# Kernel tuning notes

Measured on AMD Instinct MI355X. Metric: run time of the kernel, lower is better.

Reference implementation:

```python
import jax, jax.numpy as jnp
import numpy as np

N_HEAD = 4
D_MODEL = 128
D_K = D_MODEL // N_HEAD
N = 65536


def setup_inputs() -> dict:
    key = jax.random.key(0)
    ks = jax.random.split(key, 9)
    s = 1.0 / np.sqrt(D_MODEL)
    return {
        "query": jax.random.normal(ks[0], (N, D_MODEL), jnp.float32),
        "key": jax.random.normal(ks[1], (N, D_MODEL), jnp.float32),
        "value": jax.random.normal(ks[2], (N, D_MODEL), jnp.float32),
        "Wq": jax.random.normal(ks[3], (D_MODEL, D_MODEL), jnp.float32) * s,
        "bq": jax.random.normal(ks[4], (D_MODEL,), jnp.float32) * s,
        "Wk": jax.random.normal(ks[5], (D_MODEL, D_MODEL), jnp.float32) * s,
        "bk": jax.random.normal(ks[6], (D_MODEL,), jnp.float32) * s,
        "Wv": jax.random.normal(ks[7], (D_MODEL, D_MODEL), jnp.float32) * s,
        "bv": jax.random.normal(ks[8], (D_MODEL,), jnp.float32) * s,
    }


def _proj(x, W, b):
    # nn.Linear: x @ W.T + b, then view(N, n_head, d_k).transpose(0, 1) -> (h, N, d_k)
    y = x @ W.T + b
    return jnp.transpose(y.reshape(-1, N_HEAD, D_K), (1, 0, 2))


def reference(query, key, value, Wq, bq, Wk, bk, Wv, bv):
    n = query.shape[0]
    q = _proj(query, Wq, bq)  # (h, N, d_k)
    k = _proj(key, Wk, bk)
    v = _proj(value, Wv, bv)
    # galerkin linear attention: p_attn = (K^T V) / seq_len, out = Q @ p_attn
    p_attn = jnp.einsum("hnd,hne->hde", k, v) / n  # (h, d_k, d_k)
    x = jnp.einsum("hnd,hde->hne", q, p_attn)  # (h, N, d_k)
    # faithful to x.transpose(1,2).contiguous().view(bsz, -1, n_head*d_k)
    att_output = jnp.transpose(x, (0, 2, 1)).reshape(n, -1, N_HEAD * D_K)  # (N, 1, d_model)
    return att_output, p_attn
```

## Files before the change

kernel.cpp:

```cpp
#include <hip/hip_runtime.h>

typedef __attribute__((ext_vector_type(8))) short short8;
typedef __attribute__((ext_vector_type(4))) float f32x4;

#define WS_CKV  0
#define WS_SKEY 16384
#define WS_SVAL 16512
#define WS_W2T  16640
#define WS_B2   24832

#define SCR_CS  4194304

__device__ inline ushort f2bf(float f) {
    uint u = __float_as_uint(f);
    return (ushort)((u + 0x7FFFu + ((u >> 16) & 1u)) >> 16);
}
__device__ inline uint pack_bf16(float a, float b) {
    return (uint)f2bf(a) | ((uint)f2bf(b) << 16);
}
__device__ inline float bf2f(ushort u) { return __uint_as_float(((uint)u) << 16); }

__global__ __launch_bounds__(512, 4) void kernelA(const float* __restrict__ key,
                                                  const float* __restrict__ value,
                                                  float* __restrict__ outbuf) {
    __shared__ float lk[2][32 * 128];
    __shared__ float lv[2][32 * 128];
    __shared__ float red[256];

    const int tid = threadIdx.x;
    const int i0 = (tid >> 5) * 8;
    const int j0 = (tid & 31) * 4;
    const int row0 = blockIdx.x * 128;

    const float4* __restrict__ k4 = (const float4*)key;
    const float4* __restrict__ v4 = (const float4*)value;

    float acc[8][4];
#pragma unroll
    for (int a = 0; a < 8; ++a)
#pragma unroll
        for (int b = 0; b < 4; ++b) acc[a][b] = 0.f;

    float sk[4] = {0.f, 0.f, 0.f, 0.f};
    float sv[4] = {0.f, 0.f, 0.f, 0.f};

    float4 rk[2], rv[2];
    {
        const int g = row0 * 32;
        rk[0] = k4[g + tid]; rk[1] = k4[g + tid + 512];
        rv[0] = v4[g + tid]; rv[1] = v4[g + tid + 512];
        ((float4*)lk[0])[tid] = rk[0]; ((float4*)lk[0])[tid + 512] = rk[1];
        ((float4*)lv[0])[tid] = rv[0]; ((float4*)lv[0])[tid + 512] = rv[1];
#pragma unroll
        for (int q = 0; q < 2; ++q) {
            sk[0] += rk[q].x; sk[1] += rk[q].y; sk[2] += rk[q].z; sk[3] += rk[q].w;
            sv[0] += rv[q].x; sv[1] += rv[q].y; sv[2] += rv[q].z; sv[3] += rv[q].w;
        }
    }
    __syncthreads();

    for (int t = 0; t < 4; ++t) {
        const int cur = t & 1;
        if (t < 3) {
            const int g = (row0 + (t + 1) * 32) * 32;
            rk[0] = k4[g + tid]; rk[1] = k4[g + tid + 512];
            rv[0] = v4[g + tid]; rv[1] = v4[g + tid + 512];
        }
#pragma unroll 4
        for (int kk = 0; kk < 32; ++kk) {
            float ka[8], vb[4];
            *(float4*)&ka[0] = *(const float4*)&lk[cur][kk * 128 + i0];
            *(float4*)&ka[4] = *(const float4*)&lk[cur][kk * 128 + i0 + 4];
            *(float4*)&vb[0] = *(const float4*)&lv[cur][kk * 128 + j0];
#pragma unroll
            for (int a = 0; a < 8; ++a)
#pragma unroll
                for (int b = 0; b < 4; ++b)
                    acc[a][b] = fmaf(ka[a], vb[b], acc[a][b]);
        }
        if (t < 3) {
            const int nxt = cur ^ 1;
            ((float4*)lk[nxt])[tid] = rk[0]; ((float4*)lk[nxt])[tid + 512] = rk[1];
            ((float4*)lv[nxt])[tid] = rv[0]; ((float4*)lv[nxt])[tid + 512] = rv[1];
#pragma unroll
            for (int q = 0; q < 2; ++q) {
                sk[0] += rk[q].x; sk[1] += rk[q].y; sk[2] += rk[q].z; sk[3] += rk[q].w;
                sv[0] += rv[q].x; sv[1] += rv[q].y; sv[2] += rv[q].z; sv[3] += rv[q].w;
            }
            __syncthreads();
        }
    }

    if (tid < 256) red[tid] = 0.f;
    __syncthreads();
    const int cg = (tid & 31) * 4;
#pragma unroll
    for (int a = 0; a < 4; ++a) {
        atomicAdd(&red[cg + a], sk[a]);
        atomicAdd(&red[128 + cg + a], sv[a]);
    }
    __syncthreads();

    ushort* __restrict__ tile = (ushort*)outbuf + (size_t)blockIdx.x * 16384;
#pragma unroll
    for (int a = 0; a < 8; ++a) {
        uint2 s;
        s.x = pack_bf16(acc[a][0], acc[a][1]);
        s.y = pack_bf16(acc[a][2], acc[a][3]);
        *(uint2*)&tile[(i0 + a) * 128 + j0] = s;
    }
    if (tid < 256) outbuf[SCR_CS + blockIdx.x * 256 + tid] = red[tid];
}

__global__ __launch_bounds__(512) void kernelR(const float* __restrict__ outbuf,
                                               float* __restrict__ ws) {
    __shared__ float red[8][64];
    const int tid = threadIdx.x;
    const int b = blockIdx.x;
    const int lane = tid & 63;
    const int g = tid >> 6;
    const int p0 = g * 64;

    float s[8];
#pragma unroll
    for (int c = 0; c < 8; ++c) s[c] = 0.f;

    if (b < 256) {
        const ushort* __restrict__ tile = (const ushort*)outbuf;
        const int e = b * 64 + lane;
        for (int r = 0; r < 8; ++r) {
#pragma unroll
            for (int c = 0; c < 8; ++c)
                s[c] += bf2f(tile[(size_t)(p0 + c * 8 + r) * 16384 + e]);
        }
    } else {
        const int e = (b - 256) * 64 + lane;
        for (int r = 0; r < 8; ++r) {
#pragma unroll
            for (int c = 0; c < 8; ++c)
                s[c] += outbuf[SCR_CS + (p0 + c * 8 + r) * 256 + e];
        }
    }
    red[g][lane] = ((s[0] + s[1]) + (s[2] + s[3])) + ((s[4] + s[5]) + (s[6] + s[7]));
    __syncthreads();
    if (tid < 64) {
        float r = ((red[0][lane] + red[1][lane]) + (red[2][lane] + red[3][lane])) +
                  ((red[4][lane] + red[5][lane]) + (red[6][lane] + red[7][lane]));
        if (b < 256) ws[b * 64 + lane] = r;
        else ws[WS_SKEY + (b - 256) * 64 + lane] = r;
    }
}

__global__ __launch_bounds__(512) void kernelB(const float* __restrict__ Wk, const float* __restrict__ bk,
                                               const float* __restrict__ Wv, const float* __restrict__ bv,
                                               const float* __restrict__ Wq, const float* __restrict__ bq,
                                               float* __restrict__ ws, float* __restrict__ out) {
    __shared__ float ckv[128 * 132];
    __shared__ float wvT[128 * 32];
    __shared__ float wk_s[32 * 132];
    __shared__ float wq_s[32 * 132];
    __shared__ float Tl[128 * 32];
    __shared__ float pl[32 * 32];
    __shared__ float skey[128], sval[128];
    __shared__ float bk_s[32], bv_s[32], bq_s[32];
    __shared__ float wvec[32], uvec[32];

    const int tid = threadIdx.x;
    const int h = blockIdx.x;

    const float4* __restrict__ ws4 = (const float4*)ws;
    const float4* __restrict__ Wk4 = (const float4*)Wk;
    const float4* __restrict__ Wq4 = (const float4*)Wq;
    const float4* __restrict__ Wv4 = (const float4*)Wv;

#pragma unroll
    for (int q = 0; q < 8; ++q) {
        const int idx = tid + 512 * q;
        float4 v = ws4[(WS_CKV >> 2) + idx];
        *(float4*)&ckv[(idx >> 5) * 132 + (idx & 31) * 4] = v;
    }
#pragma unroll
    for (int q = 0; q < 2; ++q) {
        const int idx = tid + 512 * q;
        float4 a = Wk4[h * 1024 + idx];
        float4 b = Wq4[h * 1024 + idx];
        *(float4*)&wk_s[(idx >> 5) * 132 + (idx & 31) * 4] = a;
        *(float4*)&wq_s[(idx >> 5) * 132 + (idx & 31) * 4] = b;
    }
#pragma unroll
    for (int q = 0; q < 2; ++q) {
        const int f = tid + 512 * q;
        const int e = f >> 5;
        const int c = (f & 31) * 4;
        float4 v = Wv4[h * 1024 + f];
        wvT[(c + 0) * 32 + e] = v.x;
        wvT[(c + 1) * 32 + e] = v.y;
        wvT[(c + 2) * 32 + e] = v.z;
        wvT[(c + 3) * 32 + e] = v.w;
    }
    if (tid < 128) { skey[tid] = ws[WS_SKEY + tid]; sval[tid] = ws[WS_SVAL + tid]; }
    else if (tid >= 256 && tid < 288) {
        const int u = tid - 256;
        bk_s[u] = bk[h * 32 + u]; bv_s[u] = bv[h * 32 + u]; bq_s[u] = bq[h * 32 + u];
    }
    __syncthreads();

    {
        const int i = tid >> 2;
        const int e0 = (tid & 3) * 8;
        float accT8[8];
#pragma unroll
        for (int e = 0; e < 8; ++e) accT8[e] = 0.f;
        for (int j = 0; j < 128; ++j) {
            const float cv = ckv[i * 132 + j];
            const float* wr = &wvT[j * 32 + e0];
#pragma unroll
            for (int e = 0; e < 8; ++e) accT8[e] = fmaf(cv, wr[e], accT8[e]);
        }
#pragma unroll
        for (int e = 0; e < 8; e += 4)
            *(float4*)&Tl[i * 32 + e0 + e] = make_float4(accT8[e], accT8[e+1], accT8[e+2], accT8[e+3]);

        if (tid < 32) {
            float u = 0.f;
            for (int j = 0; j < 128; ++j) u = fmaf(wvT[j * 32 + tid], sval[j], u);
            uvec[tid] = u;
        } else if (tid < 64) {
            const int a = tid - 32;
            float w = 0.f;
            for (int i2 = 0; i2 < 128; ++i2) w = fmaf(wk_s[a * 132 + i2], skey[i2], w);
            wvec[a] = w;
        }
    }
    __syncthreads();

    {
        const int d = tid >> 4;
        const int e2 = (tid & 15) * 2;
        float pa = 0.f, pb = 0.f;
        for (int i2 = 0; i2 < 128; ++i2) {
            const float wkv = wk_s[d * 132 + i2];
            pa = fmaf(wkv, Tl[i2 * 32 + e2], pa);
            pb = fmaf(wkv, Tl[i2 * 32 + e2 + 1], pb);
        }
        const float p0 = (pa + wvec[d] * bv_s[e2] + bk_s[d] * uvec[e2] +
                          65536.f * bk_s[d] * bv_s[e2]) * (1.f / 65536.f);
        const float p1 = (pb + wvec[d] * bv_s[e2 + 1] + bk_s[d] * uvec[e2 + 1] +
                          65536.f * bk_s[d] * bv_s[e2 + 1]) * (1.f / 65536.f);
        pl[d * 32 + e2] = p0; pl[d * 32 + e2 + 1] = p1;
        *(float2*)&out[8388608 + h * 1024 + d * 32 + e2] = make_float2(p0, p1);
    }
    __syncthreads();

    {
        const int k = tid >> 2;
        const int e0 = (tid & 3) * 8;
        float accW[8];
#pragma unroll
        for (int e = 0; e < 8; ++e) accW[e] = 0.f;
        for (int d = 0; d < 32; ++d) {
            const float wq = wq_s[d * 132 + k];
            const float* pr = &pl[d * 32 + e0];
#pragma unroll
            for (int e = 0; e < 8; ++e) accW[e] = fmaf(wq, pr[e], accW[e]);
        }
        ushort* __restrict__ w2t = (ushort*)(ws + WS_W2T);
#pragma unroll
        for (int e = 0; e < 8; ++e)
            w2t[(h * 32 + e0 + e) * 128 + k] = f2bf(accW[e]);

        if (tid < 32) {
            float b2v = 0.f;
#pragma unroll
            for (int d = 0; d < 32; ++d) b2v = fmaf(bq_s[d], pl[d * 32 + tid], b2v);
            ws[WS_B2 + h * 32 + tid] = b2v;
        }
    }
}

__global__ __launch_bounds__(256, 2) void kernelC(const float* __restrict__ query,
                                                  const float* __restrict__ ws,
                                                  float* __restrict__ out) {
    __shared__ __align__(16) ushort qs[128 * 136];
    __shared__ __align__(16) ushort w2s[128 * 136];
    __shared__ float b2s[128];

    const int tid = threadIdx.x;
    const int lane = tid & 63;
    const int w = tid >> 6;
    const int wr = w >> 1, wc = w & 1;
    const int rowbase = blockIdx.x * 128;

    {
        const float4* __restrict__ q4 = (const float4*)query;
        const int r = tid >> 1, half = tid & 1;
        const int gbase = (rowbase + r) * 32 + half * 16;
#pragma unroll
        for (int m = 0; m < 8; ++m) {
            float4 f0 = q4[gbase + m * 2], f1 = q4[gbase + m * 2 + 1];
            uint4 pk;
            pk.x = pack_bf16(f0.x, f0.y); pk.y = pack_bf16(f0.z, f0.w);
            pk.z = pack_bf16(f1.x, f1.y); pk.w = pack_bf16(f1.z, f1.w);
            *(uint4*)&qs[r * 136 + half * 64 + m * 8] = pk;
        }
    }
    {
        const uint4* __restrict__ wsrc = (const uint4*)((const ushort*)(ws + WS_W2T));
        const int c = tid >> 1, half = tid & 1;
#pragma unroll
        for (int m = 0; m < 8; ++m) {
            uint4 v = wsrc[c * 16 + half * 8 + m];
            *(uint4*)&w2s[c * 136 + half * 64 + m * 8] = v;
        }
    }
    if (tid < 32) ((float4*)b2s)[tid] = ((const float4*)(ws + WS_B2))[tid];
    __syncthreads();

    short8 bfrag[4][4];
#pragma unroll
    for (int ct = 0; ct < 4; ++ct)
#pragma unroll
        for (int ks = 0; ks < 4; ++ks)
            bfrag[ct][ks] = *(const short8*)&w2s[(wc * 64 + ct * 16 + (lane & 15)) * 136 + ks * 32 + (lane >> 4) * 8];

    f32x4 acc[4][4];
#pragma unroll
    for (int rt = 0; rt < 4; ++rt)
#pragma unroll
        for (int ct = 0; ct < 4; ++ct) acc[rt][ct] = (f32x4){0.f, 0.f, 0.f, 0.f};

#pragma unroll
    for (int ks = 0; ks < 4; ++ks) {
        short8 af[4];
#pragma unroll
        for (int rt = 0; rt < 4; ++rt)
            af[rt] = *(const short8*)&qs[(wr * 64 + rt * 16 + (lane & 15)) * 136 + ks * 32 + (lane >> 4) * 8];
#pragma unroll
        for (int rt = 0; rt < 4; ++rt)
#pragma unroll
            for (int ct = 0; ct < 4; ++ct)
                acc[rt][ct] = __builtin_amdgcn_mfma_f32_16x16x32_bf16(af[rt], bfrag[ct][ks], acc[rt][ct], 0, 0, 0);
    }
    __syncthreads();

    float* tmp = (float*)qs;
#pragma unroll
    for (int cp = 0; cp < 4; ++cp) {
        if (wc == (cp >> 1)) {
#pragma unroll
            for (int rt = 0; rt < 4; ++rt)
#pragma unroll
                for (int tc = 0; tc < 2; ++tc) {
                    const int ct = (cp & 1) * 2 + tc;
                    const int cl = tc * 16 + (lane & 15);
                    const int r = wr * 64 + rt * 16 + (lane >> 4) * 4;
                    *(f32x4*)&tmp[cl * 132 + r] = acc[rt][ct];
                }
        }
        __syncthreads();
        {
            const int cl = tid >> 3;
            const int c = cp * 32 + cl;
            const float bb = b2s[c];
            float* __restrict__ col = out + (size_t)c * 65536 + rowbase;
#pragma unroll
            for (int ch = 0; ch < 4; ++ch) {
                const int r4 = (tid & 7) + ch * 8;
                float4 v = *(const float4*)&tmp[cl * 132 + r4 * 4];
                v.x += bb; v.y += bb; v.z += bb; v.w += bb;
                *(float4*)&col[r4 * 4] = v;
            }
        }
        __syncthreads();
    }
}

extern "C" void kernel_launch(void* const* d_in, const int* in_sizes, int n_in,
                              void* d_out, int out_size, void* d_ws, size_t ws_size,
                              hipStream_t stream) {
    const float* query = (const float*)d_in[0];
    const float* key   = (const float*)d_in[1];
    const float* value = (const float*)d_in[2];
    const float* Wq = (const float*)d_in[3];
    const float* bq = (const float*)d_in[4];
    const float* Wk = (const float*)d_in[5];
    const float* bk = (const float*)d_in[6];
    const float* Wv = (const float*)d_in[7];
    const float* bv = (const float*)d_in[8];
    float* out = (float*)d_out;
    float* ws  = (float*)d_ws;

    hipLaunchKernelGGL(kernelA, dim3(512), dim3(512), 0, stream, key, value, out);
    hipLaunchKernelGGL(kernelR, dim3(260), dim3(512), 0, stream, out, ws);
    hipLaunchKernelGGL(kernelB, dim3(4), dim3(512), 0, stream, Wk, bk, Wv, bv, Wq, bq, ws, out);
    hipLaunchKernelGGL(kernelC, dim3(512), dim3(256), 0, stream, query, ws, out);
}
```

Before: 197.4 us.

## Use bf16 MFMA for K^T V partial sums and coalesce staging loads

The per-block K^T·V partial products in kernelA now use bf16 MFMA 16x16x32 instead of scalar fp32 FMAs. K and V tiles are converted to bf16 and stored transposed in swizzled shared memory. The output tile is staged through shared memory so the global writes are coalesced uint4 stores. KernelC's query and weight loads into LDS are reorganized so consecutive threads read consecutive global addresses. This lowers ALU work and improves memory coalescing, at the cost of rounding K and V to bf16 before accumulation.

```diff
diff --git a/kernel.cpp b/kernel.cpp
--- a/kernel.cpp
+++ b/kernel.cpp
@@ -23,38 +23,48 @@
 __global__ __launch_bounds__(512, 4) void kernelA(const float* __restrict__ key,
                                                   const float* __restrict__ value,
                                                   float* __restrict__ outbuf) {
-    __shared__ float lk[2][32 * 128];
-    __shared__ float lv[2][32 * 128];
+    __shared__ __align__(16) ushort sm[4][128 * 40];
     __shared__ float red[256];
 
     const int tid = threadIdx.x;
-    const int i0 = (tid >> 5) * 8;
-    const int j0 = (tid & 31) * 4;
+    const int l = tid & 63;
+    const int w = tid >> 6;
+    const int rs = w * 16;
     const int row0 = blockIdx.x * 128;
 
     const float4* __restrict__ k4 = (const float4*)key;
     const float4* __restrict__ v4 = (const float4*)value;
 
-    float acc[8][4];
-#pragma unroll
-    for (int a = 0; a < 8; ++a)
-#pragma unroll
-        for (int b = 0; b < 4; ++b) acc[a][b] = 0.f;
+    const int n2 = tid >> 5;
+    const int i4 = tid & 31;
+    const int i0 = i4 * 4;
+    const int nds = n2 ^ (((i4 >> 1) & 3) << 2);
+
+    const int lr = l & 15;
+    const int g = l >> 4;
+
+    f32x4 acc[8];
+#pragma unroll
+    for (int c = 0; c < 8; ++c) acc[c] = (f32x4){0.f, 0.f, 0.f, 0.f};
 
     float sk[4] = {0.f, 0.f, 0.f, 0.f};
     float sv[4] = {0.f, 0.f, 0.f, 0.f};
 
-    float4 rk[2], rv[2];
-    {
-        const int g = row0 * 32;
-        rk[0] = k4[g + tid]; rk[1] = k4[g + tid + 512];
-        rv[0] = v4[g + tid]; rv[1] = v4[g + tid + 512];
-        ((float4*)lk[0])[tid] = rk[0]; ((float4*)lk[0])[tid + 512] = rk[1];
-        ((float4*)lv[0])[tid] = rv[0]; ((float4*)lv[0])[tid + 512] = rv[1];
-#pragma unroll
-        for (int q = 0; q < 2; ++q) {
-            sk[0] += rk[q].x; sk[1] += rk[q].y; sk[2] += rk[q].z; sk[3] += rk[q].w;
-            sv[0] += rv[q].x; sv[1] += rv[q].y; sv[2] += rv[q].z; sv[3] += rv[q].w;
+    float4 rka, rkb, rva, rvb;
+    {
+        const int gb = (row0 + 2 * n2) * 32 + i4;
+        rka = k4[gb]; rkb = k4[gb + 32];
+        rva = v4[gb]; rvb = v4[gb + 32];
+        uint* dk = (uint*)sm[0];
+        uint* dv = (uint*)sm[1];
+        const float* pa = (const float*)&rka; const float* pb = (const float*)&rkb;
+        const float* pc = (const float*)&rva; const float* pd = (const float*)&rvb;
+#pragma unroll
+        for (int q = 0; q < 4; ++q) {
+            dk[(i0 + q) * 20 + nds] = pack_bf16(pa[q], pb[q]);
+            dv[(i0 + q) * 20 + nds] = pack_bf16(pc[q], pd[q]);
+            sk[q] += pa[q] + pb[q];
+            sv[q] += pc[q] + pd[q];
         }
     }
     __syncthreads();
@@ -62,30 +72,36 @@
     for (int t = 0; t < 4; ++t) {
         const int cur = t & 1;
         if (t < 3) {
-            const int g = (row0 + (t + 1) * 32) * 32;
-            rk[0] = k4[g + tid]; rk[1] = k4[g + tid + 512];
-            rv[0] = v4[g + tid]; rv[1] = v4[g + tid + 512];
-        }
-#pragma unroll 4
-        for (int kk = 0; kk < 32; ++kk) {
-            float ka[8], vb[4];
-            *(float4*)&ka[0] = *(const float4*)&lk[cur][kk * 128 + i0];
-            *(float4*)&ka[4] = *(const float4*)&lk[cur][kk * 128 + i0 + 4];
-            *(float4*)&vb[0] = *(const float4*)&lv[cur][kk * 128 + j0];
-#pragma unroll
-            for (int a = 0; a < 8; ++a)
-#pragma unroll
-                for (int b = 0; b < 4; ++b)
-                    acc[a][b] = fmaf(ka[a], vb[b], acc[a][b]);
+            const int gb = (row0 + (t + 1) * 32 + 2 * n2) * 32 + i4;
+            rka = k4[gb]; rkb = k4[gb + 32];
+            rva = v4[gb]; rvb = v4[gb + 32];
+        }
+        {
+            const ushort* sK = sm[cur * 2 + 0];
+            const ushort* sV = sm[cur * 2 + 1];
+            const int ia = rs + lr;
+            const int ga = g ^ ((ia >> 3) & 3);
+            short8 af = *(const short8*)(sK + ia * 40 + ga * 8);
+#pragma unroll
+            for (int c = 0; c < 8; ++c) {
+                const int ib = c * 16 + lr;
+                const int gb2 = g ^ ((ib >> 3) & 3);
+                short8 bf = *(const short8*)(sV + ib * 40 + gb2 * 8);
+                acc[c] = __builtin_amdgcn_mfma_f32_16x16x32_bf16(af, bf, acc[c], 0, 0, 0);
+            }
         }
         if (t < 3) {
             const int nxt = cur ^ 1;
-            ((float4*)lk[nxt])[tid] = rk[0]; ((float4*)lk[nxt])[tid + 512] = rk[1];
-            ((float4*)lv[nxt])[tid] = rv[0]; ((float4*)lv[nxt])[tid + 512] = rv[1];
-#pragma unroll
-            for (int q = 0; q < 2; ++q) {
-                sk[0] += rk[q].x; sk[1] += rk[q].y; sk[2] += rk[q].z; sk[3] += rk[q].w;
-                sv[0] += rv[q].x; sv[1] += rv[q].y; sv[2] += rv[q].z; sv[3] += rv[q].w;
+            uint* dk = (uint*)sm[nxt * 2 + 0];
+            uint* dv = (uint*)sm[nxt * 2 + 1];
+            const float* pa = (const float*)&rka; const float* pb = (const float*)&rkb;
+            const float* pc = (const float*)&rva; const float* pd = (const float*)&rvb;
+#pragma unroll
+            for (int q = 0; q < 4; ++q) {
+                dk[(i0 + q) * 20 + nds] = pack_bf16(pa[q], pb[q]);
+                dv[(i0 + q) * 20 + nds] = pack_bf16(pc[q], pd[q]);
+                sk[q] += pa[q] + pb[q];
+                sv[q] += pc[q] + pd[q];
             }
             __syncthreads();
         }
@@ -93,21 +109,28 @@
 
     if (tid < 256) red[tid] = 0.f;
     __syncthreads();
-    const int cg = (tid & 31) * 4;
-#pragma unroll
-    for (int a = 0; a < 4; ++a) {
-        atomicAdd(&red[cg + a], sk[a]);
-        atomicAdd(&red[128 + cg + a], sv[a]);
+#pragma unroll
+    for (int q = 0; q < 4; ++q) {
+        atomicAdd(&red[i0 + q], sk[q]);
+        atomicAdd(&red[128 + i0 + q], sv[q]);
+    }
+
+    ushort* sc = sm[0];
+#pragma unroll
+    for (int c = 0; c < 8; ++c) {
+        const float* av = (const float*)&acc[c];
+#pragma unroll
+        for (int r = 0; r < 4; ++r)
+            sc[(rs + g * 4 + r) * 136 + c * 16 + lr] = f2bf(av[r]);
     }
     __syncthreads();
 
     ushort* __restrict__ tile = (ushort*)outbuf + (size_t)blockIdx.x * 16384;
 #pragma unroll
-    for (int a = 0; a < 8; ++a) {
-        uint2 s;
-        s.x = pack_bf16(acc[a][0], acc[a][1]);
-        s.y = pack_bf16(acc[a][2], acc[a][3]);
-        *(uint2*)&tile[(i0 + a) * 128 + j0] = s;
+    for (int q2 = 0; q2 < 4; ++q2) {
+        const int id = tid + 512 * q2;
+        const int r = id >> 4, p = id & 15;
+        ((uint4*)tile)[id] = *(const uint4*)(sc + r * 136 + p * 8);
     }
     if (tid < 256) outbuf[SCR_CS + blockIdx.x * 256 + tid] = red[tid];
 }
@@ -292,25 +315,26 @@
     const int rowbase = blockIdx.x * 128;
 
     {
-        const float4* __restrict__ q4 = (const float4*)query;
-        const int r = tid >> 1, half = tid & 1;
-        const int gbase = (rowbase + r) * 32 + half * 16;
-#pragma unroll
-        for (int m = 0; m < 8; ++m) {
-            float4 f0 = q4[gbase + m * 2], f1 = q4[gbase + m * 2 + 1];
-            uint4 pk;
-            pk.x = pack_bf16(f0.x, f0.y); pk.y = pack_bf16(f0.z, f0.w);
-            pk.z = pack_bf16(f1.x, f1.y); pk.w = pack_bf16(f1.z, f1.w);
-            *(uint4*)&qs[r * 136 + half * 64 + m * 8] = pk;
+        const float4* __restrict__ q4 = (const float4*)query + (size_t)rowbase * 32;
+        uint2* __restrict__ qd = (uint2*)qs;
+#pragma unroll
+        for (int it = 0; it < 16; ++it) {
+            const int idx = tid + 256 * it;
+            float4 f = q4[idx];
+            const int r = idx >> 5, c4 = idx & 31;
+            uint2 pk;
+            pk.x = pack_bf16(f.x, f.y);
+            pk.y = pack_bf16(f.z, f.w);
+            qd[r * 34 + c4] = pk;
         }
     }
     {
         const uint4* __restrict__ wsrc = (const uint4*)((const ushort*)(ws + WS_W2T));
-        const int c = tid >> 1, half = tid & 1;
-#pragma unroll
-        for (int m = 0; m < 8; ++m) {
-            uint4 v = wsrc[c * 16 + half * 8 + m];
-            *(uint4*)&w2s[c * 136 + half * 64 + m * 8] = v;
+        uint4* __restrict__ wd = (uint4*)w2s;
+#pragma unroll
+        for (int q = 0; q < 8; ++q) {
+            const int idx = tid + 256 * q;
+            wd[(idx >> 4) * 17 + (idx & 15)] = wsrc[idx];
         }
     }
     if (tid < 32) ((float4*)b2s)[tid] = ((const float4*)(ws + WS_B2))[tid];
```

New measurement: 178.7 us. 1.1x faster.
